# Kernel tuning notes

Measured on AMD Instinct MI355X. Metric: run time of the kernel, lower is better.

## Reference

```python
import jax, jax.numpy as jnp
import numpy as np

D_MODEL = 512
N_HEADS = 8
HIDDEN = 2048  # mlp_ratio * d_model
B, N = 2, 1024

# 2^dim sign-flip frames for FrameAveraging(dim=2)
_FRAME_OPS = jnp.array([[1., 1.], [1., -1.], [-1., 1.], [-1., -1.]], jnp.float32)


def _ln(x, g, b, eps=1e-5):
    mu = jnp.mean(x, axis=-1, keepdims=True)
    var = jnp.mean((x - mu) ** 2, axis=-1, keepdims=True)
    return (x - mu) * jax.lax.rsqrt(var + eps) * g + b


def setup_inputs() -> dict:
    key = jax.random.key(0)
    ks = jax.random.split(key, 8)
    s = 0.02
    return {
        "token_embs": jax.random.normal(ks[0], (B, N, D_MODEL), jnp.float32),
        "coords": jax.random.normal(ks[1], (B, N, 2), jnp.float32),
        "padding_mask": jnp.zeros((B, N, N), jnp.bool_),
        "ln1_g": jnp.ones((D_MODEL,), jnp.float32),
        "ln1_b": jnp.zeros((D_MODEL,), jnp.float32),
        "w_qkv": jax.random.normal(ks[2], (D_MODEL, 3 * D_MODEL), jnp.float32) * s,
        "b_qkv": jnp.zeros((3 * D_MODEL,), jnp.float32),
        "w_edge": jax.random.normal(ks[3], (3, N_HEADS), jnp.float32) * s,
        "w_out": jax.random.normal(ks[4], (D_MODEL, D_MODEL), jnp.float32) * s,
        "b_out": jnp.zeros((D_MODEL,), jnp.float32),
        "ln2_g": jnp.ones((D_MODEL,), jnp.float32),
        "ln2_b": jnp.zeros((D_MODEL,), jnp.float32),
        "w1": jax.random.normal(ks[5], (D_MODEL, HIDDEN), jnp.float32) * s,
        "b1": jnp.zeros((HIDDEN,), jnp.float32),
        "w2": jax.random.normal(ks[6], (HIDDEN, D_MODEL), jnp.float32) * s,
        "b2": jnp.zeros((D_MODEL,), jnp.float32),
    }


def _block(x, coords, pad_mask, ln1_g, ln1_b, w_qkv, b_qkv, w_edge, w_out, b_out,
           ln2_g, ln2_b, w1, b1, w2, b2):
    Bb, Nn, C = x.shape
    H = w_edge.shape[1]
    d = C // H
    scale = d ** -0.5
    nf = _FRAME_OPS.shape[0]

    # ---- attention QKV ----
    qkv = _ln(x, ln1_g, ln1_b) @ w_qkv + b_qkv
    q, k, v = jnp.split(qkv, 3, axis=-1)
    q = q.reshape(Bb, Nn, H, d).transpose(0, 2, 1, 3) * scale  # (B,H,N,d)
    k = k.reshape(Bb, Nn, H, d).transpose(0, 2, 1, 3)
    v = v.reshape(Bb, Nn, H, d).transpose(0, 2, 1, 3)
    attn = jnp.einsum('bhnd,bhmd->bhnm', q, k)

    # ---- pairwise radial coords + frame averaging ----
    rc = coords[:, :, None, :] - coords[:, None, :, :]           # (B,N,N,2)
    rnorm = jnp.linalg.norm(rc, axis=-1).reshape(Bb * Nn, Nn, 1)
    rc = rc.reshape(Bb * Nn, Nn, 2)                              # (M,N,2)
    valid = (~pad_mask).reshape(Bb * Nn, Nn)
    m = valid.astype(rc.dtype)[..., None]                        # (M,N,1)
    center = jnp.sum(rc * m, axis=1) / jnp.sum(m, axis=1)        # masked mean
    Xc = (rc - center[:, None]) * m                              # (M,N,2)
    Cov = jnp.einsum('mni,mnj->mij', Xc, Xc)                     # (M,2,2)
    _, V = jnp.linalg.eigh(jax.lax.stop_gradient(Cov))           # PCA frame (detached)
    F_ops = _FRAME_OPS[None, :, None, :] * V[:, None]            # (M,nf,2,2) sign-flipped eigvecs
    h = jnp.einsum('moji,mpj->mopi', F_ops, Xc) * m[:, None]     # (M,nf,N,2)

    feat = jnp.concatenate(
        [h, jnp.broadcast_to(rnorm[:, None], (Bb * Nn, nf, Nn, 1))], axis=-1)  # (M,nf,N,3)
    bias = jnp.einsum('monk,kh->monh', feat, w_edge).mean(axis=1)  # (M,N,H)
    bias = bias.reshape(Bb, Nn, Nn, H).transpose(0, 3, 1, 2)       # (B,H,N,N)

    attn = attn + bias
    attn = jnp.where(pad_mask[:, None], jnp.float32(-1e9), attn)
    attn = jax.nn.softmax(attn, axis=-1)
    o = jnp.einsum('bhnm,bhmd->bhnd', attn, v)
    o = o.transpose(0, 2, 1, 3).reshape(Bb, Nn, C) @ w_out + b_out

    x = x + o
    y = _ln(x, ln2_g, ln2_b)
    y = jax.nn.gelu(y @ w1 + b1, approximate=False) @ w2 + b2
    return x + y


def reference(token_embs, coords, padding_mask, ln1_g, ln1_b, w_qkv, b_qkv, w_edge,
              w_out, b_out, ln2_g, ln2_b, w1, b1, w2, b2):
    return _block(token_embs, coords, padding_mask, ln1_g, ln1_b, w_qkv, b_qkv,
                  w_edge, w_out, b_out, ln2_g, ln2_b, w1, b1, w2, b2)
```

## Files before the change

kernel.cpp:

```cpp
#include <hip/hip_runtime.h>
#include <hip/hip_bf16.h>
#include <math.h>

#define NHEADS 8
#define NTOK   1024
#define MTOK   2048

typedef __attribute__((ext_vector_type(8))) short  sh8;
typedef __attribute__((ext_vector_type(8))) __bf16 bf16x8;
typedef __attribute__((ext_vector_type(4))) float  f32x4;
typedef __attribute__((ext_vector_type(4))) unsigned int u32x4;

__device__ __forceinline__ short f2bf(float v) {
    return __builtin_bit_cast(short, __float2bfloat16(v));
}
__device__ __forceinline__ float bf2f(short v) {
    return __builtin_bit_cast(float, ((unsigned)(unsigned short)v) << 16);
}
__device__ __forceinline__ float ex2(float v) {
    return __builtin_amdgcn_exp2f(v);
}
__device__ __forceinline__ f32x4 mfma16(sh8 a, sh8 b, f32x4 c) {
    return __builtin_amdgcn_mfma_f32_16x16x32_bf16(
        __builtin_bit_cast(bf16x8, a), __builtin_bit_cast(bf16x8, b), c, 0, 0, 0);
}
__device__ __forceinline__ void aload16(void* lds, const void* g) {
    __builtin_amdgcn_global_load_lds(
        (const __attribute__((address_space(1))) unsigned int*)g,
        (__attribute__((address_space(3))) unsigned int*)lds, 16, 0, 0);
}

#define LOG2E 1.4426950408889634f

__global__ __launch_bounds__(256) void ln_bf16(const float* __restrict__ x,
    const float* __restrict__ g, const float* __restrict__ bta, short* __restrict__ y)
{
    int row = blockIdx.x, t = threadIdx.x;
    const float* xr = x + (size_t)row * 512;
    float2 v = *reinterpret_cast<const float2*>(&xr[t*2]);
    float s = v.x + v.y, ss = v.x*v.x + v.y*v.y;
    #pragma unroll
    for (int m = 1; m < 64; m <<= 1) { s += __shfl_xor(s, m); ss += __shfl_xor(ss, m); }
    __shared__ float red[8];
    int wid = t >> 6, lane = t & 63;
    if (!lane) { red[wid] = s; red[4+wid] = ss; }
    __syncthreads();
    s = red[0]+red[1]+red[2]+red[3]; ss = red[4]+red[5]+red[6]+red[7];
    float mu = s*(1.f/512), var = ss*(1.f/512) - mu*mu, rs = rsqrtf(var + 1e-5f);
    float2 gg = *reinterpret_cast<const float2*>(&g[t*2]);
    float2 bb = *reinterpret_cast<const float2*>(&bta[t*2]);
    short2 o; o.x = f2bf((v.x-mu)*rs*gg.x + bb.x); o.y = f2bf((v.y-mu)*rs*gg.y + bb.y);
    *reinterpret_cast<short2*>(&y[(size_t)row*512 + t*2]) = o;
}

__global__ __launch_bounds__(256) void wconv2x(
    const float* __restrict__ W0, short* __restrict__ WT0, int K0, int N0, int nb0,
    const float* __restrict__ W1, short* __restrict__ WT1, int K1, int N1)
{
    const float* W; short* WT; int K, N, bid;
    if ((int)blockIdx.x < nb0) { W = W0; WT = WT0; K = K0; N = N0; bid = blockIdx.x; }
    else                       { W = W1; WT = WT1; K = K1; N = N1; bid = blockIdx.x - nb0; }
    int nbx = N >> 5;
    int bn = (bid % nbx) * 32, bk = (bid / nbx) * 32;
    __shared__ float t[32][33];
    int c = threadIdx.x & 31, r8 = threadIdx.x >> 5;
    #pragma unroll
    for (int i = 0; i < 4; ++i) {
        int r = r8 + i*8;
        t[r][c] = W[(size_t)(bk + r)*N + bn + c];
    }
    __syncthreads();
    #pragma unroll
    for (int i = 0; i < 4; ++i) {
        int r = r8 + i*8;
        WT[(size_t)(bn + r)*K + bk + c] = f2bf(t[c][r]);
    }
}

__global__ __launch_bounds__(256) void prep(const float* __restrict__ coords,
    const unsigned char* __restrict__ mask, short* __restrict__ rnP,
    unsigned long long* __restrict__ mbP)
{
    __shared__ float2 kc_s[64];
    __shared__ float2 qc_s[16];
    int bid = blockIdx.x;
    int bqt = bid >> 4, jt = bid & 15;
    int b = bqt >> 6, qt = bqt & 63;
    int t = threadIdx.x, w = t >> 6, lane = t & 63;
    int lr = lane & 15, lg = lane >> 4;

    if (t < 64)            kc_s[t]      = *reinterpret_cast<const float2*>(&coords[(size_t)(b*1024 + jt*64 + t)*2]);
    else if (t < 80)       qc_s[t - 64] = *reinterpret_cast<const float2*>(&coords[(size_t)(b*1024 + qt*16 + (t - 64))*2]);
    __syncthreads();

    float2 qc = qc_s[lr];
    short4 o;
    short* op = &o.x;
    #pragma unroll
    for (int r = 0; r < 4; ++r) {
        float2 kc = kc_s[w*16 + lg*4 + r];
        float dx = qc.x - kc.x, dy = qc.y - kc.y;
        op[r] = f2bf(sqrtf(dx*dx + dy*dy));
    }
    *reinterpret_cast<short4*>(&rnP[(size_t)((bid*4 + w)*256) + lane*4]) = o;

    #pragma unroll
    for (int i = 0; i < 4; ++i) {
        int q = w*4 + i;
        unsigned char v = mask[(size_t)(b*1024 + qt*16 + q)*NTOK + jt*64 + lane];
        unsigned long long bits = __ballot(v != 0);
        if (!lane) mbP[(size_t)bid*16 + q] = bits;
    }
}

template<int EPI, bool OUTBF, bool BIAS_ROW, bool QSC, int NT>
__global__ __launch_bounds__(256) void gemm64(
    const short* __restrict__ A, const short* __restrict__ BT,
    const float* __restrict__ bias, const float* __restrict__ res,
    void* __restrict__ Cout, int M, int N, int K, int nbx)
{
    __shared__ sh8 As8[3][512];
    __shared__ sh8 Bs8[3][512];
    int tid = threadIdx.x;
    int w = tid >> 6, lane = tid & 63, lr = lane & 15, lg = lane >> 4;
    int wr = w >> 1, wc = w & 1;
    int cpx = gridDim.x >> 3;
    int swz = (blockIdx.x & 7)*cpx + (blockIdx.x >> 3);
    int bx = swz % nbx, by = swz / nbx;
    int bm0 = by*64, bn0 = bx*64;

    f32x4 zero = {0.f,0.f,0.f,0.f};
    f32x4 acc[2][2];
    #pragma unroll
    for (int m = 0; m < 2; ++m)
        #pragma unroll
        for (int n = 0; n < 2; ++n) acc[m][n] = zero;

    #define STAGE(buf, k0) { \
        _Pragma("unroll") \
        for (int it = 0; it < 2; ++it) { \
            int s = tid + it*256; \
            int r = s >> 3, g = s & 7; \
            int ksw = (k0) + ((g ^ (r & 7)) << 3); \
            aload16(&As8[buf][s], A  + (size_t)(bm0 + r)*K + ksw); \
            aload16(&Bs8[buf][s], BT + (size_t)(bn0 + r)*K + ksw); \
        } }

    STAGE(0, 0)
    if (NT > 1) STAGE(1, 64)

    #pragma unroll
    for (int t = 0; t < NT; ++t) {
        if (t + 1 < NT) asm volatile("s_waitcnt vmcnt(4)" ::: "memory");
        else            asm volatile("s_waitcnt vmcnt(0)" ::: "memory");
        __builtin_amdgcn_s_barrier();
        __builtin_amdgcn_sched_barrier(0);
        int buf = t % 3;
        sh8 af[2][2], bfv[2][2];
        #pragma unroll
        for (int m = 0; m < 2; ++m) {
            int R = wr*32 + m*16 + lr;
            #pragma unroll
            for (int s = 0; s < 2; ++s) af[m][s] = As8[buf][R*8 + ((s*4+lg) ^ (R & 7))];
        }
        #pragma unroll
        for (int n = 0; n < 2; ++n) {
            int R = wc*32 + n*16 + lr;
            #pragma unroll
            for (int s = 0; s < 2; ++s) bfv[n][s] = Bs8[buf][R*8 + ((s*4+lg) ^ (R & 7))];
        }
        if (t + 2 < NT) STAGE((t+2)%3, (t+2)*64)
        #pragma unroll
        for (int m = 0; m < 2; ++m)
            #pragma unroll
            for (int n = 0; n < 2; ++n)
                #pragma unroll
                for (int s = 0; s < 2; ++s)
                    acc[m][n] = mfma16(af[m][s], bfv[n][s], acc[m][n]);
        asm volatile("s_waitcnt lgkmcnt(0)" ::: "memory");
    }
    #undef STAGE

    #pragma unroll
    for (int m = 0; m < 2; ++m) {
        #pragma unroll
        for (int n = 0; n < 2; ++n) {
            #pragma unroll
            for (int r = 0; r < 4; ++r) {
                int row = bm0 + wr*32 + m*16 + lg*4 + r;
                int col = bn0 + wc*32 + n*16 + lr;
                float v = acc[m][n][r] + (BIAS_ROW ? bias[row] : bias[col]);
                if (QSC && col < 512) v *= (0.125f * LOG2E);
                if (EPI == 1) v += res[(size_t)row*N + col];
                if (EPI == 2) v = 0.5f * v * (1.0f + erff(v * 0.70710678f));
                if (OUTBF) ((short*)Cout)[(size_t)row*N + col] = f2bf(v);
                else       ((float*)Cout)[(size_t)row*N + col] = v;
            }
        }
    }
}

template<int EPI, bool OUTBF, bool BIAS_ROW, int NT>
__global__ __launch_bounds__(256) void gemm32n(
    const short* __restrict__ A, const short* __restrict__ BT,
    const float* __restrict__ bias, const float* __restrict__ res,
    void* __restrict__ Cout, int M, int N, int K, int nbx)
{
    __shared__ sh8 As8[3][512];
    __shared__ sh8 Bs8[3][256];
    int tid = threadIdx.x;
    int w = tid >> 6, lane = tid & 63, lr = lane & 15, lg = lane >> 4;
    int cpx = gridDim.x >> 3;
    int swz = (blockIdx.x & 7)*cpx + (blockIdx.x >> 3);
    int bx = swz % nbx, by = swz / nbx;
    int bm0 = by*64, bn0 = bx*32;

    f32x4 zero = {0.f,0.f,0.f,0.f};
    f32x4 acc[2];
    acc[0] = zero; acc[1] = zero;

    #define STAGE32(buf, k0) { \
        _Pragma("unroll") \
        for (int it = 0; it < 2; ++it) { \
            int s = tid + it*256; \
            int r = s >> 3, g = s & 7; \
            int ksw = (k0) + ((g ^ (r & 7)) << 3); \
            aload16(&As8[buf][s], A + (size_t)(bm0 + r)*K + ksw); \
        } \
        { int r = tid >> 3, g = tid & 7; \
          int ksw = (k0) + ((g ^ (r & 7)) << 3); \
          aload16(&Bs8[buf][tid], BT + (size_t)(bn0 + r)*K + ksw); } }

    STAGE32(0, 0)
    if (NT > 1) STAGE32(1, 64)

    #pragma unroll
    for (int t = 0; t < NT; ++t) {
        if (t + 1 < NT) asm volatile("s_waitcnt vmcnt(3)" ::: "memory");
        else            asm volatile("s_waitcnt vmcnt(0)" ::: "memory");
        __builtin_amdgcn_s_barrier();
        __builtin_amdgcn_sched_barrier(0);
        int buf = t % 3;
        sh8 af[2], bfv[2][2];
        int Ra = w*16 + lr;
        #pragma unroll
        for (int s = 0; s < 2; ++s) af[s] = As8[buf][Ra*8 + ((s*4+lg) ^ (Ra & 7))];
        #pragma unroll
        for (int n = 0; n < 2; ++n) {
            int R = n*16 + lr;
            #pragma unroll
            for (int s = 0; s < 2; ++s) bfv[n][s] = Bs8[buf][R*8 + ((s*4+lg) ^ (R & 7))];
        }
        if (t + 2 < NT) STAGE32((t+2)%3, (t+2)*64)
        #pragma unroll
        for (int n = 0; n < 2; ++n)
            #pragma unroll
            for (int s = 0; s < 2; ++s)
                acc[n] = mfma16(af[s], bfv[n][s], acc[n]);
        asm volatile("s_waitcnt lgkmcnt(0)" ::: "memory");
    }
    #undef STAGE32

    #pragma unroll
    for (int n = 0; n < 2; ++n) {
        #pragma unroll
        for (int r = 0; r < 4; ++r) {
            int row = bm0 + w*16 + lg*4 + r;
            int col = bn0 + n*16 + lr;
            float v = acc[n][r] + (BIAS_ROW ? bias[row] : bias[col]);
            if (EPI == 1) v += res[(size_t)row*N + col];
            if (EPI == 2) v = 0.5f * v * (1.0f + erff(v * 0.70710678f));
            if (OUTBF) ((short*)Cout)[(size_t)row*N + col] = f2bf(v);
            else       ((float*)Cout)[(size_t)row*N + col] = v;
        }
    }
}

__global__ __launch_bounds__(256) void attn_reg(
    const short* __restrict__ qk, const short* __restrict__ vt,
    const short* __restrict__ rnP, const unsigned long long* __restrict__ mbP,
    const float* __restrict__ w_edge, short* __restrict__ OpA,
    short* __restrict__ OpB, float* __restrict__ ml)
{
    __shared__ sh8 Ks8[2][512];
    __shared__ sh8 Vs8[2][512];

    int cpx = gridDim.x >> 3;
    int swz = (blockIdx.x & 7)*cpx + (blockIdx.x >> 3);
    int w = threadIdx.x >> 6, lane = threadIdx.x & 63;
    int lr = lane & 15, lg = lane >> 4;
    int qb = swz & 15;
    int h  = (swz >> 4) & 7;
    int b  = (swz >> 7) & 1;
    int ks = swz >> 8;

    const int q0 = qb*64 + w*16;
    const int qrow0 = b*NTOK + q0;
    const int jt0 = ks*4;
    const int bqt = b*64 + qb*4 + w;

    sh8 qf[2];
    #pragma unroll
    for (int s = 0; s < 2; ++s)
        qf[s] = *reinterpret_cast<const sh8*>(qk + (size_t)(qrow0 + lr)*1024 + h*64 + s*32 + lg*8);

    float we2l = w_edge[2*NHEADS + h] * LOG2E;

    float m_i = -1e30f, l_lane = 0.f;
    f32x4 zero = {0.f,0.f,0.f,0.f};
    f32x4 accO[4];
    #pragma unroll
    for (int n = 0; n < 4; ++n) accO[n] = zero;

    const short* kbase = qk + 512 + h*64;
    const short* vbase = vt + (size_t)h*64*2048 + b*NTOK;
    int sr = threadIdx.x >> 3, sg = threadIdx.x & 7;
    int sx = (sg ^ (sr & 7)) << 3;

    #define ASTAGE(bf, jt) { \
        aload16(&Ks8[bf][threadIdx.x],       kbase + (size_t)(b*NTOK + (jt)*64 + sr)*1024 + sx); \
        aload16(&Ks8[bf][threadIdx.x + 256], kbase + (size_t)(b*NTOK + (jt)*64 + sr + 32)*1024 + sx); \
        aload16(&Vs8[bf][threadIdx.x],       vbase + (size_t)sr*2048 + (jt)*64 + sx); \
        aload16(&Vs8[bf][threadIdx.x + 256], vbase + (size_t)(sr + 32)*2048 + (jt)*64 + sx); \
    }

    short4 rn_reg[2][4];
    unsigned long long mr_reg[2];
    #define RMLOAD(bf, jt) { \
        _Pragma("unroll") \
        for (int n = 0; n < 4; ++n) \
            rn_reg[bf][n] = *reinterpret_cast<const short4*>( \
                &rnP[(size_t)(((bqt*16 + (jt))*4 + n)*256) + lane*4]); \
        mr_reg[bf] = mbP[(size_t)(bqt*16 + (jt))*16 + lr]; \
    }

    ASTAGE(0, jt0)
    RMLOAD(0, jt0)

    #pragma unroll
    for (int t = 0; t < 4; ++t) {
        if (t == 0) asm volatile("s_waitcnt vmcnt(0)" ::: "memory");
        else        asm volatile("s_waitcnt vmcnt(5)" ::: "memory");
        __builtin_amdgcn_s_barrier();
        __builtin_amdgcn_sched_barrier(0);
        int buf = t & 1;

        if (t + 1 < 4) {
            ASTAGE(buf ^ 1, jt0 + t + 1)
            RMLOAD(buf ^ 1, jt0 + t + 1)
        }

        f32x4 Sv[4];
        #pragma unroll
        for (int n = 0; n < 4; ++n) {
            int kcol = n*16 + lr;
            sh8 k0v = Ks8[buf][kcol*8 + (lg       ^ (kcol & 7))];
            sh8 k1v = Ks8[buf][kcol*8 + ((4 + lg) ^ (kcol & 7))];
            Sv[n] = mfma16(k1v, qf[1], mfma16(k0v, qf[0], zero));
        }

        #pragma unroll
        for (int n = 0; n < 4; ++n) {
            short4 rn4 = rn_reg[buf][n];
            Sv[n][0] = fmaf(bf2f(rn4.x), we2l, Sv[n][0]);
            Sv[n][1] = fmaf(bf2f(rn4.y), we2l, Sv[n][1]);
            Sv[n][2] = fmaf(bf2f(rn4.z), we2l, Sv[n][2]);
            Sv[n][3] = fmaf(bf2f(rn4.w), we2l, Sv[n][3]);
        }

        float mx = Sv[0][0];
        #pragma unroll
        for (int n = 0; n < 4; ++n)
            #pragma unroll
            for (int r = 0; r < 4; ++r) mx = fmaxf(mx, Sv[n][r]);
        mx = fmaxf(mx, __shfl_xor(mx, 16));
        mx = fmaxf(mx, __shfl_xor(mx, 32));

        if (!__all(mx <= m_i + 8.0f)) {
            float mnew = fmaxf(m_i, mx);
            float f = ex2(m_i - mnew);
            m_i = mnew;
            l_lane *= f;
            float fb[4];
            #pragma unroll
            for (int r = 0; r < 4; ++r) fb[r] = __shfl(f, lg*4 + r);
            #pragma unroll
            for (int n = 0; n < 4; ++n)
                #pragma unroll
                for (int r = 0; r < 4; ++r) accO[n][r] *= fb[r];
        }

        unsigned long long mr = mr_reg[buf];
        float ps = 0.f;
        unsigned pk[8];
        #pragma unroll
        for (int n = 0; n < 4; ++n) {
            float p_[4];
            #pragma unroll
            for (int r = 0; r < 4; ++r) {
                float p = ex2(Sv[n][r] - m_i);
                p = ((mr >> (n*16 + lg*4 + r)) & 1ull) ? 0.f : p;
                ps += p;
                p_[r] = p;
            }
            asm("v_cvt_pk_bf16_f32 %0, %1, %2" : "=v"(pk[2*n])   : "v"(p_[0]), "v"(p_[1]));
            asm("v_cvt_pk_bf16_f32 %0, %1, %2" : "=v"(pk[2*n+1]) : "v"(p_[2]), "v"(p_[3]));
        }
        l_lane += ps;

        int src0 = lr + ((lg & 1) << 5);
        int src1 = src0 + 16;
        sh8 pa[2];
        #pragma unroll
        for (int s = 0; s < 2; ++s) {
            int ns = 2*s + (lg >> 1);
            u32x4 dv;
            dv.x = (unsigned)__shfl((int)pk[2*ns],   src0);
            dv.y = (unsigned)__shfl((int)pk[2*ns+1], src0);
            dv.z = (unsigned)__shfl((int)pk[2*ns],   src1);
            dv.w = (unsigned)__shfl((int)pk[2*ns+1], src1);
            pa[s] = __builtin_bit_cast(sh8, dv);
        }

        #pragma unroll
        for (int n = 0; n < 4; ++n) {
            int dcol = n*16 + lr;
            sh8 v0 = Vs8[buf][dcol*8 + (lg       ^ (dcol & 7))];
            sh8 v1 = Vs8[buf][dcol*8 + ((4 + lg) ^ (dcol & 7))];
            accO[n] = mfma16(pa[1], v1, mfma16(pa[0], v0, accO[n]));
        }

        asm volatile("s_waitcnt lgkmcnt(0)" ::: "memory");
    }
    #undef ASTAGE
    #undef RMLOAD

    l_lane += __shfl_xor(l_lane, 16);
    l_lane += __shfl_xor(l_lane, 32);

    short* Op = (ks < 2) ? OpA : OpB;
    #pragma unroll
    for (int r = 0; r < 4; ++r) {
        size_t row = (size_t)((ks & 1)*MTOK + qrow0 + lg*4 + r);
        #pragma unroll
        for (int n = 0; n < 4; ++n)
            Op[row*512 + h*64 + n*16 + lr] = f2bf(accO[n][r]);
    }
    if (lg == 0) {
        size_t mrow = (size_t)(ks*MTOK + qrow0 + lr);
        ml[(mrow*NHEADS + h)*2 + 0] = m_i;
        ml[(mrow*NHEADS + h)*2 + 1] = l_lane;
    }
}

__global__ __launch_bounds__(256) void attn_combine4(const short* __restrict__ OpA,
    const short* __restrict__ OpB, const float* __restrict__ ml,
    short* __restrict__ ob)
{
    int idx = blockIdx.x*256 + threadIdx.x;
    int tok = idx >> 7, dd = (idx & 127) * 4;
    int h = dd >> 6;
    float m[4], l[4];
    #pragma unroll
    for (int s = 0; s < 4; ++s) {
        m[s] = ml[(((size_t)s*MTOK + tok)*NHEADS + h)*2 + 0];
        l[s] = ml[(((size_t)s*MTOK + tok)*NHEADS + h)*2 + 1];
    }
    float mm = fmaxf(fmaxf(m[0], m[1]), fmaxf(m[2], m[3]));
    float wsum = 0.f, a0 = 0.f, a1 = 0.f, a2 = 0.f, a3 = 0.f;
    #pragma unroll
    for (int s = 0; s < 4; ++s) {
        float wv = ex2(m[s] - mm);
        wsum += wv * l[s];
        const short* Op = (s < 2) ? OpA : OpB;
        short4 p = *reinterpret_cast<const short4*>(&Op[((size_t)((s&1)*MTOK) + tok)*512 + dd]);
        a0 += bf2f(p.x)*wv; a1 += bf2f(p.y)*wv;
        a2 += bf2f(p.z)*wv; a3 += bf2f(p.w)*wv;
    }
    float inv = 1.f / wsum;
    short4 o;
    o.x = f2bf(a0*inv); o.y = f2bf(a1*inv);
    o.z = f2bf(a2*inv); o.w = f2bf(a3*inv);
    *reinterpret_cast<short4*>(&ob[(size_t)tok*512 + dd]) = o;
}

extern "C" void kernel_launch(void* const* d_in, const int* in_sizes, int n_in,
                              void* d_out, int out_size, void* d_ws, size_t ws_size,
                              hipStream_t stream)
{
    const float* x      = (const float*)d_in[0];
    const float* coords = (const float*)d_in[1];
    const unsigned char* mask = (const unsigned char*)d_in[2];
    const float* ln1_g = (const float*)d_in[3];
    const float* ln1_b = (const float*)d_in[4];
    const float* w_qkv = (const float*)d_in[5];
    const float* b_qkv = (const float*)d_in[6];
    const float* w_edge= (const float*)d_in[7];
    const float* w_out = (const float*)d_in[8];
    const float* b_out = (const float*)d_in[9];
    const float* ln2_g = (const float*)d_in[10];
    const float* ln2_b = (const float*)d_in[11];
    const float* w1    = (const float*)d_in[12];
    const float* b1    = (const float*)d_in[13];
    const float* w2    = (const float*)d_in[14];
    const float* b2    = (const float*)d_in[15];
    float* out = (float*)d_out;

    char* W = (char*)d_ws;
    const size_t MB = 1024*1024;
    float* x1    = (float*)(W);
    short* qk    = (short*)(W + 4*MB);
    short* vtb   = (short*)(W + 8*MB);
    short* woutT = (short*)(W + 10*MB);
    short* xln   = (short*)(W + 10*MB + 512*1024);
    short* wqkvT = (short*)(W + 12*MB + 512*1024);
    short* OpB   = (short*)(W + 10*MB + 512*1024);
    short* OpA   = (short*)(W + 14*MB + 512*1024);
    short* rnP   = (short*)(W + 18*MB + 512*1024);
    float* mlp   = (float*)(W + 22*MB + 512*1024);
    unsigned long long* mbP = (unsigned long long*)(W + 23*MB);
    short* ob    = (short*)(W + 6*MB);
    short* y     = xln;
    short* w1T   = (short*)(W + 4*MB);
    short* w2T   = (short*)(W + 8*MB);
    short* hid   = (short*)(W + 14*MB + 512*1024);

    prep<<<dim3(2048,1,1), 256, 0, stream>>>(coords, mask, rnP, mbP);
    wconv2x<<<dim3(1024,1,1), 256, 0, stream>>>(w_qkv, wqkvT, 512, 1536, 768,
                                                w_out, woutT, 512, 512);
    ln_bf16<<<MTOK, 256, 0, stream>>>(x, ln1_g, ln1_b, xln);
    gemm64<0,true,false,true,8><<<dim3(512,1,1), 256, 0, stream>>>(
        xln, wqkvT, b_qkv, nullptr, qk, MTOK, 1024, 512, 16);
    gemm32n<0,true,true,8><<<dim3(512,1,1), 256, 0, stream>>>(
        wqkvT + (size_t)1024*512, xln, b_qkv + 1024, nullptr, vtb, 512, MTOK, 512, 64);
    attn_reg<<<dim3(1024,1,1), 256, 0, stream>>>(qk, vtb, rnP, mbP, w_edge, OpA, OpB, mlp);
    attn_combine4<<<dim3(1024,1,1), 256, 0, stream>>>(OpA, OpB, mlp, ob);
    gemm32n<1,false,false,8><<<dim3(512,1,1), 256, 0, stream>>>(
        ob, woutT, b_out, x, x1, MTOK, 512, 512, 16);
    wconv2x<<<dim3(2048,1,1), 256, 0, stream>>>(w1, w1T, 512, 2048, 1024,
                                                w2, w2T, 2048, 512);
    ln_bf16<<<MTOK, 256, 0, stream>>>(x1, ln2_g, ln2_b, y);
    gemm64<2,true,false,false,8><<<dim3(1024,1,1), 256, 0, stream>>>(
        y, w1T, b1, nullptr, hid, MTOK, 2048, 512, 32);
    gemm32n<1,false,false,32><<<dim3(512,1,1), 256, 0, stream>>>(
        hid, w2T, b2, x1, out, MTOK, 512, 2048, 16);
}
```

Measured before the change: 92.32 us.

## Fuse V projection into QKV GEMM with transposed epilogue; widen attention blocks

The separate transposed V GEMM is removed. The QKV GEMM now covers all 1536 output columns, and tiles in the V range write a transposed bf16 output through shared memory. The attention kernel moves to 512-thread blocks that handle 128 queries each, so every block shares one K/V staging load across 8 waves and half as many blocks are launched. This saves a launch and cuts redundant K/V global loads, at the cost of a more complex epilogue and higher per-block resource use.

```diff
diff --git a/kernel.cpp b/kernel.cpp
--- a/kernel.cpp
+++ b/kernel.cpp
@@ -113,11 +113,12 @@
     }
 }
 
-template<int EPI, bool OUTBF, bool BIAS_ROW, bool QSC, int NT>
+template<int EPI, bool OUTBF, bool BIAS_ROW, bool QSC, int NT, bool VTOUT>
 __global__ __launch_bounds__(256) void gemm64(
     const short* __restrict__ A, const short* __restrict__ BT,
     const float* __restrict__ bias, const float* __restrict__ res,
-    void* __restrict__ Cout, int M, int N, int K, int nbx)
+    void* __restrict__ Cout, short* __restrict__ vtx,
+    int M, int N, int K, int nbx, int ldc)
 {
     __shared__ sh8 As8[3][512];
     __shared__ sh8 Bs8[3][512];
@@ -181,6 +182,30 @@
     }
     #undef STAGE
 
+    if (VTOUT && bn0 >= 1024) {
+        __syncthreads();
+        short* tb = (short*)&As8[0][0];
+        #pragma unroll
+        for (int m = 0; m < 2; ++m)
+            #pragma unroll
+            for (int n = 0; n < 2; ++n)
+                #pragma unroll
+                for (int r = 0; r < 4; ++r) {
+                    int row = wr*32 + m*16 + lg*4 + r;
+                    int col = wc*32 + n*16 + lr;
+                    float v = acc[m][n][r] + bias[bn0 + col];
+                    tb[col*68 + row] = f2bf(v);
+                }
+        __syncthreads();
+        int vd = tid >> 2, t0 = (tid & 3) << 4;
+        #pragma unroll
+        for (int i = 0; i < 4; ++i) {
+            short4 s4 = *reinterpret_cast<short4*>(&tb[vd*68 + t0 + i*4]);
+            *reinterpret_cast<short4*>(&vtx[(size_t)(bn0 - 1024 + vd)*2048 + bm0 + t0 + i*4]) = s4;
+        }
+        return;
+    }
+
     #pragma unroll
     for (int m = 0; m < 2; ++m) {
         #pragma unroll
@@ -191,10 +216,10 @@
                 int col = bn0 + wc*32 + n*16 + lr;
                 float v = acc[m][n][r] + (BIAS_ROW ? bias[row] : bias[col]);
                 if (QSC && col < 512) v *= (0.125f * LOG2E);
-                if (EPI == 1) v += res[(size_t)row*N + col];
+                if (EPI == 1) v += res[(size_t)row*ldc + col];
                 if (EPI == 2) v = 0.5f * v * (1.0f + erff(v * 0.70710678f));
-                if (OUTBF) ((short*)Cout)[(size_t)row*N + col] = f2bf(v);
-                else       ((float*)Cout)[(size_t)row*N + col] = v;
+                if (OUTBF) ((short*)Cout)[(size_t)row*ldc + col] = f2bf(v);
+                else       ((float*)Cout)[(size_t)row*ldc + col] = v;
             }
         }
     }
@@ -276,7 +301,7 @@
     }
 }
 
-__global__ __launch_bounds__(256) void attn_reg(
+__global__ __launch_bounds__(512) void attn_reg(
     const short* __restrict__ qk, const short* __restrict__ vt,
     const short* __restrict__ rnP, const unsigned long long* __restrict__ mbP,
     const float* __restrict__ w_edge, short* __restrict__ OpA,
@@ -289,15 +314,15 @@
     int swz = (blockIdx.x & 7)*cpx + (blockIdx.x >> 3);
     int w = threadIdx.x >> 6, lane = threadIdx.x & 63;
     int lr = lane & 15, lg = lane >> 4;
-    int qb = swz & 15;
-    int h  = (swz >> 4) & 7;
-    int b  = (swz >> 7) & 1;
-    int ks = swz >> 8;
-
-    const int q0 = qb*64 + w*16;
+    int qb = swz & 7;
+    int h  = (swz >> 3) & 7;
+    int b  = (swz >> 6) & 1;
+    int ks = swz >> 7;
+
+    const int q0 = qb*128 + w*16;
     const int qrow0 = b*NTOK + q0;
     const int jt0 = ks*4;
-    const int bqt = b*64 + qb*4 + w;
+    const int bqt = b*64 + qb*8 + w;
 
     sh8 qf[2];
     #pragma unroll
@@ -318,10 +343,8 @@
     int sx = (sg ^ (sr & 7)) << 3;
 
     #define ASTAGE(bf, jt) { \
-        aload16(&Ks8[bf][threadIdx.x],       kbase + (size_t)(b*NTOK + (jt)*64 + sr)*1024 + sx); \
-        aload16(&Ks8[bf][threadIdx.x + 256], kbase + (size_t)(b*NTOK + (jt)*64 + sr + 32)*1024 + sx); \
-        aload16(&Vs8[bf][threadIdx.x],       vbase + (size_t)sr*2048 + (jt)*64 + sx); \
-        aload16(&Vs8[bf][threadIdx.x + 256], vbase + (size_t)(sr + 32)*2048 + (jt)*64 + sx); \
+        aload16(&Ks8[bf][threadIdx.x], kbase + (size_t)(b*NTOK + (jt)*64 + sr)*1024 + sx); \
+        aload16(&Vs8[bf][threadIdx.x], vbase + (size_t)sr*2048 + (jt)*64 + sx); \
     }
 
     short4 rn_reg[2][4];
@@ -339,8 +362,7 @@
 
     #pragma unroll
     for (int t = 0; t < 4; ++t) {
-        if (t == 0) asm volatile("s_waitcnt vmcnt(0)" ::: "memory");
-        else        asm volatile("s_waitcnt vmcnt(5)" ::: "memory");
+        asm volatile("s_waitcnt vmcnt(5)" ::: "memory");
         __builtin_amdgcn_s_barrier();
         __builtin_amdgcn_sched_barrier(0);
         int buf = t & 1;
@@ -529,19 +551,17 @@
     wconv2x<<<dim3(1024,1,1), 256, 0, stream>>>(w_qkv, wqkvT, 512, 1536, 768,
                                                 w_out, woutT, 512, 512);
     ln_bf16<<<MTOK, 256, 0, stream>>>(x, ln1_g, ln1_b, xln);
-    gemm64<0,true,false,true,8><<<dim3(512,1,1), 256, 0, stream>>>(
-        xln, wqkvT, b_qkv, nullptr, qk, MTOK, 1024, 512, 16);
-    gemm32n<0,true,true,8><<<dim3(512,1,1), 256, 0, stream>>>(
-        wqkvT + (size_t)1024*512, xln, b_qkv + 1024, nullptr, vtb, 512, MTOK, 512, 64);
-    attn_reg<<<dim3(1024,1,1), 256, 0, stream>>>(qk, vtb, rnP, mbP, w_edge, OpA, OpB, mlp);
+    gemm64<0,true,false,true,8,true><<<dim3(768,1,1), 256, 0, stream>>>(
+        xln, wqkvT, b_qkv, nullptr, qk, vtb, MTOK, 1536, 512, 24, 1024);
+    attn_reg<<<dim3(512,1,1), 512, 0, stream>>>(qk, vtb, rnP, mbP, w_edge, OpA, OpB, mlp);
     attn_combine4<<<dim3(1024,1,1), 256, 0, stream>>>(OpA, OpB, mlp, ob);
     gemm32n<1,false,false,8><<<dim3(512,1,1), 256, 0, stream>>>(
         ob, woutT, b_out, x, x1, MTOK, 512, 512, 16);
     wconv2x<<<dim3(2048,1,1), 256, 0, stream>>>(w1, w1T, 512, 2048, 1024,
                                                 w2, w2T, 2048, 512);
     ln_bf16<<<MTOK, 256, 0, stream>>>(x1, ln2_g, ln2_b, y);
-    gemm64<2,true,false,false,8><<<dim3(1024,1,1), 256, 0, stream>>>(
-        y, w1T, b1, nullptr, hid, MTOK, 2048, 512, 32);
+    gemm64<2,true,false,false,8,false><<<dim3(1024,1,1), 256, 0, stream>>>(
+        y, w1T, b1, nullptr, hid, nullptr, MTOK, 2048, 512, 32, 2048);
     gemm32n<1,false,false,32><<<dim3(512,1,1), 256, 0, stream>>>(
         hid, w2T, b2, x1, out, MTOK, 512, 2048, 16);
 }
```

Result: faster. 85.41 us (-7.5%).
